# Performance work log

Hardware: AMD Instinct MI355X
Metric: run time of the kernel (lower is better)

The kernel has to match this reference:

```python
import jax, jax.numpy as jnp
import numpy as np


def setup_inputs() -> dict:
    key = jax.random.key(0)
    k1, k2 = jax.random.split(key)
    B, S, D = 4, 2048, 128
    x = jax.random.normal(k1, (B, S, D), dtype=jnp.float32)
    concept_map = jax.random.normal(k2, (D, D, D), dtype=jnp.float32) * 0.02
    return {"x": x, "concept_map": concept_map}


def reference(x, concept_map):
    # x: [B, S, D]; concept_map: [D, D, D]
    B, S, D = x.shape
    DECAY = jnp.asarray(1.2, x.dtype)

    # Decayed running sum: s_i = (s_{i-1} + x_{i-1}) / 1.2, s_0 = 0.
    def step(c, xt):
        c = (c + xt) / DECAY
        return c, c

    _, s = jax.lax.scan(step, jnp.zeros((B, D), x.dtype), jnp.swapaxes(x[:, :-1], 0, 1))
    s = jnp.swapaxes(s, 0, 1)                                   # [B, S-1, D]
    s = jnp.concatenate([jnp.zeros((B, 1, D), x.dtype), s], 1)  # [B, S, D]; step 0 contributes zeros

    # conceptual_matrix[b,s] = outer(x[b,s], s[b,s]); result[b,s,f] = sum_{d,e} cm[b,s,d,e] * W[f,d,e]
    # (dropout is identity at inference)
    return jnp.einsum('bsd,bse,fde->bsf', x, s, concept_map, optimize=True)
```

## Files before the change

kernel.cpp:

```cpp
#include <hip/hip_runtime.h>

typedef _Float16 f16;
typedef _Float16 f16x2 __attribute__((ext_vector_type(2)));
typedef _Float16 f16x8 __attribute__((ext_vector_type(8)));
typedef float f32x16 __attribute__((ext_vector_type(16)));
typedef unsigned int u32;
typedef unsigned int u32x4 __attribute__((ext_vector_type(4)));

static __device__ __forceinline__ u32 pk2(float lo, float hi) {
  union { f16 h[2]; u32 u; } v;
  v.h[0] = (f16)lo; v.h[1] = (f16)hi;
  return v.u;
}

__global__ void k_pre(const float* __restrict__ W, char* __restrict__ wt,
                      const float* __restrict__ x, float* __restrict__ st) {
  int bid = blockIdx.x;
  if (bid < 2048) {
    int t = bid * 256 + threadIdx.x;
    long i = (long)t * 4;
    int f = (int)(i >> 14);
    int k = (int)(i & 16383);
    float4 w4 = *(const float4*)(W + i);
    int d = k >> 7, e = k & 127;
    long byo = (long)d * 32768 + (e >> 5) * 8192 + f * 64 + ((e >> 3) & 3) * 16 + (e & 7) * 2;
    u32* dst = (u32*)(wt + byo);
    dst[0] = pk2(w4.x, w4.y);
    dst[1] = pk2(w4.z, w4.w);
  } else {
    int tid = (bid - 2048) * 256 + threadIdx.x;
    int e  = tid & 127;
    int bc = tid >> 7;
    int b  = bc >> 5;
    int ch = bc & 31;
    int t0 = ch * 64;
    const float* xb = x + (long)b * 2048 * 128 + e;
    float* sb = st + (long)e * 8192 + b * 2048;
    const float inv = 1.0f / 1.2f;
    float c = 0.f;
    if (ch > 0) {
      const float* xp = xb + (long)(t0 - 64) * 128;
      #pragma unroll
      for (int t = 0; t < 64; ++t) c = (c + xp[t * 128]) * inv;
    }
    const float* xq = xb + (long)t0 * 128;
    float* sq = sb + t0;
    #pragma unroll
    for (int t = 0; t < 64; ++t) { sq[t] = c; c = (c + xq[t * 128]) * inv; }
  }
}

__global__ void k_red(const float4* __restrict__ part, float4* __restrict__ out) {
  int i = blockIdx.x * 256 + threadIdx.x;
  float4 a = part[i];
  float4 b = part[i + 262144];
  float4 c = part[i + 524288];
  float4 d = part[i + 786432];
  out[i] = make_float4(a.x + b.x + c.x + d.x, a.y + b.y + c.y + d.y,
                       a.z + b.z + c.z + d.z, a.w + b.w + c.w + d.w);
}

__global__ __launch_bounds__(512, 2) void k_main(
    const float* __restrict__ x, const float* __restrict__ st,
    const char* __restrict__ wt, float* __restrict__ part) {
  __shared__ u32 x_lds[128 * 36];
  __shared__ float red[128 * 129];

  const int tid  = threadIdx.x;
  const int bid  = blockIdx.x;
  const int kq   = bid & 3;
  const int tt   = bid >> 2;
  const int wv   = tid >> 6;
  const int lane = tid & 63;
  const int ng   = wv & 1;
  const int ep   = wv >> 1;
  const int l31  = lane & 31;
  const int hi   = lane >> 5;
  const int tokenBase = tt * 128;

  {
    int row = tid >> 2, c0 = (tid & 3) * 8;
    const float* src = x + (long)(tokenBase + row) * 128 + kq * 32 + c0;
    float4 v0 = *(const float4*)src;
    float4 v1 = *(const float4*)(src + 4);
    u32* dst = &x_lds[row * 36 + c0];
    dst[0] = pk2(v0.x, v0.x); dst[1] = pk2(v0.y, v0.y);
    dst[2] = pk2(v0.z, v0.z); dst[3] = pk2(v0.w, v0.w);
    dst[4] = pk2(v1.x, v1.x); dst[5] = pk2(v1.y, v1.y);
    dst[6] = pk2(v1.z, v1.z); dst[7] = pk2(v1.w, v1.w);
  }

  u32 sreg[4][2][4];
  {
    #pragma unroll
    for (int m = 0; m < 4; ++m)
      #pragma unroll
      for (int kk = 0; kk < 2; ++kk)
        #pragma unroll
        for (int jj = 0; jj < 4; ++jj) {
          const float* qp = st + (long)(ep * 32 + kk * 16 + hi * 8 + 2 * jj) * 8192
                              + tokenBase + m * 32 + l31;
          sreg[m][kk][jj] = pk2(qp[0], qp[8192]);
        }
  }
  __syncthreads();

  f32x16 acc[4][2];
  #pragma unroll
  for (int m = 0; m < 4; ++m)
    #pragma unroll
    for (int n = 0; n < 2; ++n)
      #pragma unroll
      for (int q = 0; q < 16; ++q) acc[m][n][q] = 0.f;

  const char* wtq = wt + (long)(kq * 32) * 32768 + ep * 8192 + ng * 4096;
  const int lboff = l31 * 64 + hi * 16;

#define BLOAD(BUF, IT)                                                       \
  {                                                                          \
    int itc = (IT) > 31 ? 31 : (IT);                                         \
    const char* wn = wtq + (long)itc * 32768;                                \
    BUF[0][0] = *(const f16x8*)(wn + lboff);                                 \
    BUF[0][1] = *(const f16x8*)(wn + 2048 + lboff);                          \
    BUF[1][0] = *(const f16x8*)(wn + 32 + lboff);                            \
    BUF[1][1] = *(const f16x8*)(wn + 2048 + 32 + lboff);                     \
  }
#define STEP(BUF, XB, J)                                                     \
  {                                                                          \
    _Pragma("unroll")                                                        \
    for (int kk = 0; kk < 2; ++kk) {                                         \
      _Pragma("unroll")                                                      \
      for (int m = 0; m < 4; ++m) {                                          \
        f16x2 xv2;                                                           \
        *(u32*)&xv2 = XB[m][J];                                              \
        union { u32 u[4]; f16x8 v; } au;                                     \
        _Pragma("unroll")                                                    \
        for (int jj = 0; jj < 4; ++jj) {                                     \
          f16x2 s2;                                                          \
          *(u32*)&s2 = sreg[m][kk][jj];                                      \
          f16x2 p = xv2 * s2;                                                \
          au.u[jj] = *(u32*)&p;                                              \
        }                                                                    \
        acc[m][0] = __builtin_amdgcn_mfma_f32_32x32x16_f16(                  \
            au.v, BUF[kk][0], acc[m][0], 0, 0, 0);                           \
        acc[m][1] = __builtin_amdgcn_mfma_f32_32x32x16_f16(                  \
            au.v, BUF[kk][1], acc[m][1], 0, 0, 0);                           \
      }                                                                      \
    }                                                                        \
  }

  f16x8 ba[2][2], bb[2][2];
  BLOAD(ba, 0);

  #pragma unroll 1
  for (int it4 = 0; it4 < 8; ++it4) {
    u32x4 xb[4];
    #pragma unroll
    for (int m = 0; m < 4; ++m)
      xb[m] = *(const u32x4*)&x_lds[(m * 32 + l31) * 36 + it4 * 4];
    int it = it4 * 4;
    BLOAD(bb, it + 1); STEP(ba, xb, 0);
    BLOAD(ba, it + 2); STEP(bb, xb, 1);
    BLOAD(bb, it + 3); STEP(ba, xb, 2);
    BLOAD(ba, it + 4); STEP(bb, xb, 3);
  }
#undef STEP
#undef BLOAD

  __syncthreads();
  #pragma unroll
  for (int round = 0; round < 4; ++round) {
    if (ep == round) {
      #pragma unroll
      for (int m = 0; m < 4; ++m)
        #pragma unroll
        for (int n = 0; n < 2; ++n)
          #pragma unroll
          for (int reg = 0; reg < 16; ++reg) {
            int token = m * 32 + (reg & 3) + 8 * (reg >> 2) + 4 * hi;
            int idx = token * 129 + ng * 64 + n * 32 + l31;
            if (round == 0) red[idx] = acc[m][n][reg];
            else            red[idx] += acc[m][n][reg];
          }
    }
    __syncthreads();
  }
  float* outp = part + (long)kq * 1048576 + (long)tokenBase * 128;
  #pragma unroll
  for (int j = 0; j < 32; ++j) {
    int row = (tid >> 7) + j * 4;
    int col = tid & 127;
    outp[row * 128 + col] = red[row * 129 + col];
  }
}

extern "C" void kernel_launch(void* const* d_in, const int* in_sizes, int n_in,
                              void* d_out, int out_size, void* d_ws, size_t ws_size,
                              hipStream_t stream) {
  const float* x = (const float*)d_in[0];
  const float* W = (const float*)d_in[1];
  float* out  = (float*)d_out;
  float* st   = (float*)d_ws;
  char*  wt   = (char*)d_ws + (4 << 20);
  float* part = (float*)((char*)d_ws + (8 << 20));

  k_pre <<<dim3(2112), dim3(256), 0, stream>>>(W, wt, x, st);
  k_main<<<dim3(256),  dim3(512), 0, stream>>>(x, st, wt, part);
  k_red <<<dim3(1024), dim3(256), 0, stream>>>((const float4*)part, (float4*)out);
}
```

Measured before the change: 57.29 us.

## Split the contraction into eight K-slices, with two token tiles per block

Adds a templated variant where each block covers 16 of the 128 d-values (8-way split-K) and loops over two 128-token tiles. The grid stays at 256 blocks and reuses each slice's W region across both tiles. The weight-conversion block order is also permuted so writes land in a different pattern. In exchange, partial-sum traffic doubles (8 partial buffers written and reduced instead of 4), which needs more workspace. The code falls back to the 4-way path if the workspace is too small.

```diff
diff --git a/kernel.cpp b/kernel.cpp
--- a/kernel.cpp
+++ b/kernel.cpp
@@ -13,11 +13,15 @@
   return v.u;
 }
 
+template <int KLOG>
 __global__ void k_pre(const float* __restrict__ W, char* __restrict__ wt,
                       const float* __restrict__ x, float* __restrict__ st) {
   int bid = blockIdx.x;
   if (bid < 2048) {
-    int t = bid * 256 + threadIdx.x;
+    int w;
+    if (KLOG == 3) w = (bid & ~15) | (((bid & 7) << 1) | ((bid >> 3) & 1));
+    else           w = (bid & ~15) | (((bid & 3) << 2) | ((bid >> 2) & 3));
+    int t = w * 256 + threadIdx.x;
     long i = (long)t * 4;
     int f = (int)(i >> 14);
     int k = (int)(i & 16383);
@@ -50,147 +54,167 @@
   }
 }
 
+template <int KS>
 __global__ void k_red(const float4* __restrict__ part, float4* __restrict__ out) {
   int i = blockIdx.x * 256 + threadIdx.x;
-  float4 a = part[i];
-  float4 b = part[i + 262144];
-  float4 c = part[i + 524288];
-  float4 d = part[i + 786432];
-  out[i] = make_float4(a.x + b.x + c.x + d.x, a.y + b.y + c.y + d.y,
-                       a.z + b.z + c.z + d.z, a.w + b.w + c.w + d.w);
-}
-
+  float4 s = part[i];
+  #pragma unroll
+  for (int q = 1; q < KS; ++q) {
+    float4 p = part[i + (long)q * 262144];
+    s.x += p.x; s.y += p.y; s.z += p.z; s.w += p.w;
+  }
+  out[i] = s;
+}
+
+template <int KLOG>
 __global__ __launch_bounds__(512, 2) void k_main(
     const float* __restrict__ x, const float* __restrict__ st,
     const char* __restrict__ wt, float* __restrict__ part) {
-  __shared__ u32 x_lds[128 * 36];
+  constexpr int KS   = 1 << KLOG;
+  constexpr int DS   = 128 >> KLOG;
+  constexpr int NIT4 = DS / 4;
+  constexpr int XP   = DS + 4;
+  constexpr int TL   = (KLOG == 3) ? 2 : 1;
+
+  __shared__ u32 x_lds[128 * XP];
   __shared__ float red[128 * 129];
 
   const int tid  = threadIdx.x;
   const int bid  = blockIdx.x;
-  const int kq   = bid & 3;
-  const int tt   = bid >> 2;
+  const int kq   = bid & (KS - 1);
+  const int ub   = bid >> KLOG;
   const int wv   = tid >> 6;
   const int lane = tid & 63;
   const int ng   = wv & 1;
   const int ep   = wv >> 1;
   const int l31  = lane & 31;
   const int hi   = lane >> 5;
-  const int tokenBase = tt * 128;
-
-  {
-    int row = tid >> 2, c0 = (tid & 3) * 8;
-    const float* src = x + (long)(tokenBase + row) * 128 + kq * 32 + c0;
-    float4 v0 = *(const float4*)src;
-    float4 v1 = *(const float4*)(src + 4);
-    u32* dst = &x_lds[row * 36 + c0];
-    dst[0] = pk2(v0.x, v0.x); dst[1] = pk2(v0.y, v0.y);
-    dst[2] = pk2(v0.z, v0.z); dst[3] = pk2(v0.w, v0.w);
-    dst[4] = pk2(v1.x, v1.x); dst[5] = pk2(v1.y, v1.y);
-    dst[6] = pk2(v1.z, v1.z); dst[7] = pk2(v1.w, v1.w);
-  }
-
-  u32 sreg[4][2][4];
-  {
+
+  const char* wtq = wt + (long)(kq * DS) * 32768 + ep * 8192 + ng * 4096;
+  const int lboff = l31 * 64 + hi * 16;
+
+  #pragma unroll 1
+  for (int tl = 0; tl < TL; ++tl) {
+    const int tokenBase = (ub * TL + tl) * 128;
+    __syncthreads();
+
+    {
+      int row = tid >> 2, c0 = (tid & 3) * (DS / 4);
+      const float* src = x + (long)(tokenBase + row) * 128 + kq * DS + c0;
+      u32* dst = &x_lds[row * XP + c0];
+      if constexpr (DS == 32) {
+        float4 v0 = *(const float4*)src;
+        float4 v1 = *(const float4*)(src + 4);
+        dst[0] = pk2(v0.x, v0.x); dst[1] = pk2(v0.y, v0.y);
+        dst[2] = pk2(v0.z, v0.z); dst[3] = pk2(v0.w, v0.w);
+        dst[4] = pk2(v1.x, v1.x); dst[5] = pk2(v1.y, v1.y);
+        dst[6] = pk2(v1.z, v1.z); dst[7] = pk2(v1.w, v1.w);
+      } else {
+        float4 v0 = *(const float4*)src;
+        dst[0] = pk2(v0.x, v0.x); dst[1] = pk2(v0.y, v0.y);
+        dst[2] = pk2(v0.z, v0.z); dst[3] = pk2(v0.w, v0.w);
+      }
+    }
+
+    u32 sreg[4][2][4];
+    {
+      #pragma unroll
+      for (int m = 0; m < 4; ++m)
+        #pragma unroll
+        for (int kk = 0; kk < 2; ++kk)
+          #pragma unroll
+          for (int jj = 0; jj < 4; ++jj) {
+            const float* qp = st + (long)(ep * 32 + kk * 16 + hi * 8 + 2 * jj) * 8192
+                                + tokenBase + m * 32 + l31;
+            sreg[m][kk][jj] = pk2(qp[0], qp[8192]);
+          }
+    }
+    __syncthreads();
+
+    f32x16 acc[4][2];
     #pragma unroll
     for (int m = 0; m < 4; ++m)
       #pragma unroll
-      for (int kk = 0; kk < 2; ++kk)
+      for (int n = 0; n < 2; ++n)
         #pragma unroll
-        for (int jj = 0; jj < 4; ++jj) {
-          const float* qp = st + (long)(ep * 32 + kk * 16 + hi * 8 + 2 * jj) * 8192
-                              + tokenBase + m * 32 + l31;
-          sreg[m][kk][jj] = pk2(qp[0], qp[8192]);
-        }
-  }
-  __syncthreads();
-
-  f32x16 acc[4][2];
-  #pragma unroll
-  for (int m = 0; m < 4; ++m)
-    #pragma unroll
-    for (int n = 0; n < 2; ++n)
-      #pragma unroll
-      for (int q = 0; q < 16; ++q) acc[m][n][q] = 0.f;
-
-  const char* wtq = wt + (long)(kq * 32) * 32768 + ep * 8192 + ng * 4096;
-  const int lboff = l31 * 64 + hi * 16;
+        for (int q = 0; q < 16; ++q) acc[m][n][q] = 0.f;
 
 #define BLOAD(BUF, IT)                                                       \
-  {                                                                          \
-    int itc = (IT) > 31 ? 31 : (IT);                                         \
-    const char* wn = wtq + (long)itc * 32768;                                \
-    BUF[0][0] = *(const f16x8*)(wn + lboff);                                 \
-    BUF[0][1] = *(const f16x8*)(wn + 2048 + lboff);                          \
-    BUF[1][0] = *(const f16x8*)(wn + 32 + lboff);                            \
-    BUF[1][1] = *(const f16x8*)(wn + 2048 + 32 + lboff);                     \
-  }
+    {                                                                        \
+      int itc = (IT) > DS - 1 ? DS - 1 : (IT);                               \
+      const char* wn = wtq + (long)itc * 32768;                              \
+      BUF[0][0] = *(const f16x8*)(wn + lboff);                               \
+      BUF[0][1] = *(const f16x8*)(wn + 2048 + lboff);                        \
+      BUF[1][0] = *(const f16x8*)(wn + 32 + lboff);                          \
+      BUF[1][1] = *(const f16x8*)(wn + 2048 + 32 + lboff);                   \
+    }
 #define STEP(BUF, XB, J)                                                     \
-  {                                                                          \
-    _Pragma("unroll")                                                        \
-    for (int kk = 0; kk < 2; ++kk) {                                         \
+    {                                                                        \
       _Pragma("unroll")                                                      \
-      for (int m = 0; m < 4; ++m) {                                          \
-        f16x2 xv2;                                                           \
-        *(u32*)&xv2 = XB[m][J];                                              \
-        union { u32 u[4]; f16x8 v; } au;                                     \
+      for (int kk = 0; kk < 2; ++kk) {                                       \
         _Pragma("unroll")                                                    \
-        for (int jj = 0; jj < 4; ++jj) {                                     \
-          f16x2 s2;                                                          \
-          *(u32*)&s2 = sreg[m][kk][jj];                                      \
-          f16x2 p = xv2 * s2;                                                \
-          au.u[jj] = *(u32*)&p;                                              \
+        for (int m = 0; m < 4; ++m) {                                        \
+          f16x2 xv2;                                                         \
+          *(u32*)&xv2 = XB[m][J];                                            \
+          union { u32 u[4]; f16x8 v; } au;                                   \
+          _Pragma("unroll")                                                  \
+          for (int jj = 0; jj < 4; ++jj) {                                   \
+            f16x2 s2;                                                        \
+            *(u32*)&s2 = sreg[m][kk][jj];                                    \
+            f16x2 p = xv2 * s2;                                              \
+            au.u[jj] = *(u32*)&p;                                            \
+          }                                                                  \
+          acc[m][0] = __builtin_amdgcn_mfma_f32_32x32x16_f16(                \
+              au.v, BUF[kk][0], acc[m][0], 0, 0, 0);                         \
+          acc[m][1] = __builtin_amdgcn_mfma_f32_32x32x16_f16(                \
+              au.v, BUF[kk][1], acc[m][1], 0, 0, 0);                         \
         }                                                                    \
-        acc[m][0] = __builtin_amdgcn_mfma_f32_32x32x16_f16(                  \
-            au.v, BUF[kk][0], acc[m][0], 0, 0, 0);                           \
-        acc[m][1] = __builtin_amdgcn_mfma_f32_32x32x16_f16(                  \
-            au.v, BUF[kk][1], acc[m][1], 0, 0, 0);                           \
       }                                                                      \
-    }                                                                        \
-  }
-
-  f16x8 ba[2][2], bb[2][2];
-  BLOAD(ba, 0);
-
-  #pragma unroll 1
-  for (int it4 = 0; it4 < 8; ++it4) {
-    u32x4 xb[4];
-    #pragma unroll
-    for (int m = 0; m < 4; ++m)
-      xb[m] = *(const u32x4*)&x_lds[(m * 32 + l31) * 36 + it4 * 4];
-    int it = it4 * 4;
-    BLOAD(bb, it + 1); STEP(ba, xb, 0);
-    BLOAD(ba, it + 2); STEP(bb, xb, 1);
-    BLOAD(bb, it + 3); STEP(ba, xb, 2);
-    BLOAD(ba, it + 4); STEP(bb, xb, 3);
-  }
+    }
+
+    f16x8 ba[2][2], bb[2][2];
+    BLOAD(ba, 0);
+
+    #pragma unroll 1
+    for (int it4 = 0; it4 < NIT4; ++it4) {
+      u32x4 xb[4];
+      #pragma unroll
+      for (int m = 0; m < 4; ++m)
+        xb[m] = *(const u32x4*)&x_lds[(m * 32 + l31) * XP + it4 * 4];
+      int it = it4 * 4;
+      BLOAD(bb, it + 1); STEP(ba, xb, 0);
+      BLOAD(ba, it + 2); STEP(bb, xb, 1);
+      BLOAD(bb, it + 3); STEP(ba, xb, 2);
+      BLOAD(ba, it + 4); STEP(bb, xb, 3);
+    }
 #undef STEP
 #undef BLOAD
 
-  __syncthreads();
-  #pragma unroll
-  for (int round = 0; round < 4; ++round) {
-    if (ep == round) {
-      #pragma unroll
-      for (int m = 0; m < 4; ++m)
+    __syncthreads();
+    #pragma unroll
+    for (int round = 0; round < 4; ++round) {
+      if (ep == round) {
         #pragma unroll
-        for (int n = 0; n < 2; ++n)
+        for (int m = 0; m < 4; ++m)
           #pragma unroll
-          for (int reg = 0; reg < 16; ++reg) {
-            int token = m * 32 + (reg & 3) + 8 * (reg >> 2) + 4 * hi;
-            int idx = token * 129 + ng * 64 + n * 32 + l31;
-            if (round == 0) red[idx] = acc[m][n][reg];
-            else            red[idx] += acc[m][n][reg];
-          }
-    }
-    __syncthreads();
-  }
-  float* outp = part + (long)kq * 1048576 + (long)tokenBase * 128;
-  #pragma unroll
-  for (int j = 0; j < 32; ++j) {
-    int row = (tid >> 7) + j * 4;
-    int col = tid & 127;
-    outp[row * 128 + col] = red[row * 129 + col];
+          for (int n = 0; n < 2; ++n)
+            #pragma unroll
+            for (int reg = 0; reg < 16; ++reg) {
+              int token = m * 32 + (reg & 3) + 8 * (reg >> 2) + 4 * hi;
+              int idx = token * 129 + ng * 64 + n * 32 + l31;
+              if (round == 0) red[idx] = acc[m][n][reg];
+              else            red[idx] += acc[m][n][reg];
+            }
+      }
+      __syncthreads();
+    }
+    float* outp = part + (long)kq * 1048576 + (long)tokenBase * 128;
+    #pragma unroll
+    for (int j = 0; j < 32; ++j) {
+      int row = (tid >> 7) + j * 4;
+      int col = tid & 127;
+      outp[row * 128 + col] = red[row * 129 + col];
+    }
   }
 }
 
@@ -204,7 +228,14 @@
   char*  wt   = (char*)d_ws + (4 << 20);
   float* part = (float*)((char*)d_ws + (8 << 20));
 
-  k_pre <<<dim3(2112), dim3(256), 0, stream>>>(W, wt, x, st);
-  k_main<<<dim3(256),  dim3(512), 0, stream>>>(x, st, wt, part);
-  k_red <<<dim3(1024), dim3(256), 0, stream>>>((const float4*)part, (float4*)out);
-}
+  size_t need8 = (size_t)(8 << 20) + (size_t)8 * (4 << 20);
+  if (ws_size >= need8) {
+    k_pre<3><<<dim3(2112), dim3(256), 0, stream>>>(W, wt, x, st);
+    k_main<3><<<dim3(256), dim3(512), 0, stream>>>(x, st, wt, part);
+    k_red<8><<<dim3(1024), dim3(256), 0, stream>>>((const float4*)part, (float4*)out);
+  } else {
+    k_pre<2><<<dim3(2112), dim3(256), 0, stream>>>(W, wt, x, st);
+    k_main<2><<<dim3(256), dim3(512), 0, stream>>>(x, st, wt, part);
+    k_red<4><<<dim3(1024), dim3(256), 0, stream>>>((const float4*)part, (float4*)out);
+  }
+}
```

After: 72.87 us. 1.27x slower.
